# Performance work log

Hardware: AMD Instinct MI355X
Metric: run time of the kernel (lower is better)

## Reference

```python
import jax, jax.numpy as jnp
import numpy as np
from jax.ops import segment_sum

N_NODES = 100000
IN_C, HID_C, OUT_C = 128, 128, 64
N_EDGES = 1600000


def gcn_conv(x, row, col, dinv, W, b):
    # PyG GCNConv: symmetric normalization with self-loops.
    # h = X W; out[c] = sum_{(r,c) in E} dinv[r]*dinv[c]*h[r] + dinv[v]^2*h[v] + b
    h = x @ W  # [N, F_out]
    norm = dinv[row] * dinv[col]  # [E]
    agg = segment_sum(h[row] * norm[:, None], col, num_segments=x.shape[0])
    agg = agg + h * (dinv * dinv)[:, None]  # self-loop contribution
    return agg + b


def setup_inputs() -> dict:
    key = jax.random.key(0)
    k1, k2, k3, k4, k5, k6 = jax.random.split(key, 6)
    x = jax.random.normal(k1, (N_NODES, IN_C), dtype=jnp.float32)
    edge_index = jax.random.randint(k2, (2, N_EDGES), 0, N_NODES, dtype=jnp.int64)
    # Glorot-style init for GCN weights, zero bias (as in PyG GCNConv)
    W1 = jax.random.normal(k3, (IN_C, HID_C), dtype=jnp.float32) / np.sqrt(IN_C)
    b1 = jnp.zeros((HID_C,), dtype=jnp.float32)
    W2 = jax.random.normal(k4, (HID_C, OUT_C), dtype=jnp.float32) / np.sqrt(HID_C)
    b2 = jnp.zeros((OUT_C,), dtype=jnp.float32)
    return {"x": x, "edge_index": edge_index, "W1": W1, "b1": b1, "W2": W2, "b2": b2}


def reference(x, edge_index, W1, b1, W2, b2):
    row, col = edge_index[0], edge_index[1]
    n = x.shape[0]
    # degree counts include self-loop (+1)
    deg = segment_sum(jnp.ones_like(col, dtype=x.dtype), col, num_segments=n) + 1.0
    dinv = jax.lax.rsqrt(deg)
    h = gcn_conv(x, row, col, dinv, W1, b1)
    h = jax.nn.relu(h)
    # dropout is identity in eval mode (get_embedding runs model.eval())
    out = gcn_conv(h, row, col, dinv, W2, b2)
    return out
```

## Files before the change

### kernel.cpp

```cpp
#include <hip/hip_runtime.h>
#include <math.h>


#define BS 256
#define EPB 4096
#define BK_SHIFT 9

typedef __attribute__((ext_vector_type(8))) short bf16x8;
typedef __attribute__((ext_vector_type(4))) float f32x4;

union FragU {
    bf16x8 v;
    unsigned u[4];
};

__device__ __forceinline__ unsigned pack_bf16x2(float a, float b) {
    unsigned ua = __float_as_uint(a);
    unsigned ub = __float_as_uint(b);
    ua = (ua + 0x7fffu + ((ua >> 16) & 1u)) >> 16;
    ub = (ub + 0x7fffu + ((ub >> 16) & 1u)) >> 16;
    return ua | (ub << 16);
}

__device__ __forceinline__ ushort bf16_rte(float a) {
    unsigned ua = __float_as_uint(a);
    return (ushort)((ua + 0x7fffu + ((ua >> 16) & 1u)) >> 16);
}

__device__ __forceinline__ float bf_lo(unsigned u) { return __uint_as_float(u << 16); }
__device__ __forceinline__ float bf_hi(unsigned u) { return __uint_as_float(u & 0xffff0000u); }

__global__ __launch_bounds__(BS) void p1_hist_kernel(const int* __restrict__ col,
                                                     int* __restrict__ countsT,
                                                     int E, int NBUCK, int NBLK) {
    __shared__ int h[256];
    int tid = threadIdx.x;
    h[tid] = 0;
    __syncthreads();
    int e0 = blockIdx.x * EPB;
    int e1 = min(e0 + EPB, E);
    for (int i = e0 + tid; i < e1; i += BS) atomicAdd(&h[col[i] >> BK_SHIFT], 1);
    __syncthreads();
    for (int b = tid; b < NBUCK; b += BS) countsT[b * NBLK + blockIdx.x] = h[b];
}

__global__ __launch_bounds__(BS) void scan_block_kernel(const int* __restrict__ in,
                                                        int* __restrict__ exc,
                                                        int* __restrict__ bsum, int N) {
    __shared__ int s[BS];
    int tid = threadIdx.x;
    int i = blockIdx.x * BS + tid;
    int v = (i < N) ? in[i] : 0;
    s[tid] = v;
    __syncthreads();
    for (int off = 1; off < BS; off <<= 1) {
        int t = (tid >= off) ? s[tid - off] : 0;
        __syncthreads();
        s[tid] += t;
        __syncthreads();
    }
    if (i < N) exc[i] = s[tid] - v;
    if (tid == BS - 1) bsum[blockIdx.x] = s[BS - 1];
}

__global__ __launch_bounds__(512) void scan_bsum_kernel(const int* __restrict__ bsum,
                                                        int* __restrict__ boff, int NB) {
    __shared__ int s[512];
    int tid = threadIdx.x;
    int v = (tid < NB) ? bsum[tid] : 0;
    s[tid] = v;
    __syncthreads();
    for (int off = 1; off < 512; off <<= 1) {
        int t = (tid >= off) ? s[tid - off] : 0;
        __syncthreads();
        s[tid] += t;
        __syncthreads();
    }
    if (tid < NB) boff[tid] = s[tid] - v;
}

__global__ __launch_bounds__(BS) void add_off_kernel(int* __restrict__ exc,
                                                     const int* __restrict__ boff, int N) {
    int i = blockIdx.x * BS + threadIdx.x;
    if (i < N) exc[i] += boff[blockIdx.x];
}

__global__ __launch_bounds__(BS) void p2_scatter_kernel(const int* __restrict__ row,
                                                        const int* __restrict__ col,
                                                        const int* __restrict__ baseT,
                                                        uint2* __restrict__ pairs,
                                                        int E, int NBUCK, int NBLK) {
    __shared__ int cur[256];
    int tid = threadIdx.x;
    for (int b = tid; b < NBUCK; b += BS) cur[b] = baseT[b * NBLK + blockIdx.x];
    __syncthreads();
    int e0 = blockIdx.x * EPB;
    int e1 = min(e0 + EPB, E);
    for (int i = e0 + tid; i < e1; i += BS) {
        int c = col[i];
        int r = row[i];
        int pos = atomicAdd(&cur[c >> BK_SHIFT], 1);
        pairs[pos] = make_uint2((unsigned)r, (unsigned)c);
    }
}

__global__ __launch_bounds__(BS) void p3_build_kernel(const uint2* __restrict__ pairs,
                                                      const int* __restrict__ baseT,
                                                      int* __restrict__ off_g,
                                                      int* __restrict__ deg_g,
                                                      float* __restrict__ dinv,
                                                      int* __restrict__ src,
                                                      int E, int n, int NBUCK, int NBLK) {
    __shared__ int cnt[512];
    __shared__ int scn[512];
    __shared__ int a256[256];
    int tid = threadIdx.x;
    int b = blockIdx.x;
    int s = baseT[b * NBLK];
    int eEnd = (b == NBUCK - 1) ? E : baseT[(b + 1) * NBLK];

    cnt[tid] = 0;
    cnt[tid + 256] = 0;
    __syncthreads();
    for (int i = s + tid; i < eEnd; i += BS) {
        uint2 p = pairs[i];
        atomicAdd(&cnt[p.y & 511], 1);
    }
    __syncthreads();
    int pairsum = cnt[2 * tid] + cnt[2 * tid + 1];
    a256[tid] = pairsum;
    __syncthreads();
    for (int off = 1; off < 256; off <<= 1) {
        int t = (tid >= off) ? a256[tid - off] : 0;
        __syncthreads();
        a256[tid] += t;
        __syncthreads();
    }
    int exc = a256[tid] - pairsum;
    scn[2 * tid] = exc;
    scn[2 * tid + 1] = exc + cnt[2 * tid];
    __syncthreads();
#pragma unroll
    for (int l = tid; l < 512; l += BS) {
        int node = (b << BK_SHIFT) + l;
        if (node < n) {
            off_g[node] = s + scn[l];
            deg_g[node] = cnt[l];
            dinv[node] = rsqrtf((float)(cnt[l] + 1));
        }
    }
    __syncthreads();
#pragma unroll
    for (int l = tid; l < 512; l += BS) scn[l] += s;
    __syncthreads();
    for (int i = s + tid; i < eEnd; i += BS) {
        uint2 p = pairs[i];
        int pos = atomicAdd(&scn[p.y & 511], 1);
        src[pos] = (int)p.x;
    }
}

__global__ __launch_bounds__(BS) void wprep_kernel(const float* __restrict__ W1,
                                                   const float* __restrict__ W2,
                                                   ushort* __restrict__ wt1,
                                                   ushort* __restrict__ wt2) {
    int t = blockIdx.x * BS + threadIdx.x;
    if (t < 128 * 128) {
        int nn = t >> 7, k = t & 127;
        wt1[t] = bf16_rte(W1[k * 128 + nn]);
    }
    if (t < 64 * 128) {
        int nn = t >> 7, k = t & 127;
        wt2[t] = bf16_rte(W2[k * 64 + nn]);
    }
}

template <int NCH, bool IN_BF16>
__global__ __launch_bounds__(BS) void gemm_mfma_kernel(const void* __restrict__ Ain,
                                                       const ushort* __restrict__ WT,
                                                       const float* __restrict__ dinv,
                                                       unsigned* __restrict__ G, int n) {
    constexpr int NT = NCH / 16;
    constexpr int KP = 136;
    __shared__ ushort wlds[NCH * KP];

    int tid = threadIdx.x;
    for (int c = tid; c < NCH * 16; c += BS) {
        int nr = c >> 4, q16 = c & 15;
        *(uint4*)(wlds + nr * KP + q16 * 8) = ((const uint4*)WT)[c];
    }
    __syncthreads();

    int lane = tid & 63, wv = tid >> 6;
    int ml = lane & 15, quad = lane >> 4;
    int m = blockIdx.x * 64 + wv * 16 + ml;

    FragU b[4];
    if (m < n) {
        if (IN_BF16) {
#pragma unroll
            for (int ks = 0; ks < 4; ++ks) {
                uint4 t = ((const uint4*)Ain)[(size_t)m * 16 + ks * 4 + quad];
                b[ks].u[0] = t.x; b[ks].u[1] = t.y; b[ks].u[2] = t.z; b[ks].u[3] = t.w;
            }
        } else {
            const float4* A = (const float4*)Ain + (size_t)m * 32;
#pragma unroll
            for (int ks = 0; ks < 4; ++ks) {
                float4 p0 = A[ks * 8 + quad * 2];
                float4 p1 = A[ks * 8 + quad * 2 + 1];
                b[ks].u[0] = pack_bf16x2(p0.x, p0.y);
                b[ks].u[1] = pack_bf16x2(p0.z, p0.w);
                b[ks].u[2] = pack_bf16x2(p1.x, p1.y);
                b[ks].u[3] = pack_bf16x2(p1.z, p1.w);
            }
        }
    } else {
#pragma unroll
        for (int ks = 0; ks < 4; ++ks) {
            b[ks].u[0] = 0; b[ks].u[1] = 0; b[ks].u[2] = 0; b[ks].u[3] = 0;
        }
    }

    f32x4 acc[NT];
#pragma unroll
    for (int nt = 0; nt < NT; ++nt) {
        acc[nt][0] = 0.f; acc[nt][1] = 0.f; acc[nt][2] = 0.f; acc[nt][3] = 0.f;
    }

#pragma unroll
    for (int nt = 0; nt < NT; ++nt) {
#pragma unroll
        for (int ks = 0; ks < 4; ++ks) {
            bf16x8 a = *(const bf16x8*)(wlds + (nt * 16 + ml) * KP + ks * 32 + quad * 8);
            acc[nt] = __builtin_amdgcn_mfma_f32_16x16x32_bf16(a, b[ks].v, acc[nt], 0, 0, 0);
        }
    }

    if (m < n) {
        float dv = dinv[m];
        unsigned* grow = G + (size_t)m * (NCH / 2);
#pragma unroll
        for (int nt = 0; nt < NT; ++nt) {
            uint2 o;
            o.x = pack_bf16x2(acc[nt][0] * dv, acc[nt][1] * dv);
            o.y = pack_bf16x2(acc[nt][2] * dv, acc[nt][3] * dv);
            *(uint2*)(grow + nt * 8 + quad * 2) = o;
        }
    }
}

template <int C, bool RELU, bool OUT_BF16>
__global__ __launch_bounds__(BS) void agg_kernel(const unsigned* __restrict__ G,
                                                 const int* __restrict__ edge_off,
                                                 const int* __restrict__ cnt,
                                                 const int* __restrict__ src,
                                                 const float* __restrict__ dinv,
                                                 const float* __restrict__ bias,
                                                 void* __restrict__ out, int n) {
    constexpr int Gp = C / 8;
    constexpr int NPB = BS / Gp;
    int lane = threadIdx.x % Gp;
    int li = threadIdx.x / Gp;
    int node = blockIdx.x * NPB + li;
    if (node >= n) return;

    const uint4* G4 = (const uint4*)G;
    float acc[8];
    {
        uint4 sv = G4[(size_t)node * Gp + lane];
        acc[0] = bf_lo(sv.x); acc[1] = bf_hi(sv.x);
        acc[2] = bf_lo(sv.y); acc[3] = bf_hi(sv.y);
        acc[4] = bf_lo(sv.z); acc[5] = bf_hi(sv.z);
        acc[6] = bf_lo(sv.w); acc[7] = bf_hi(sv.w);
    }
    const int* sp = src + edge_off[node];
    int deg = cnt[node];

#define ACCUM(v)                                                               \
    acc[0] += bf_lo(v.x); acc[1] += bf_hi(v.x);                                \
    acc[2] += bf_lo(v.y); acc[3] += bf_hi(v.y);                                \
    acc[4] += bf_lo(v.z); acc[5] += bf_hi(v.z);                                \
    acc[6] += bf_lo(v.w); acc[7] += bf_hi(v.w);

    int i = 0;
    for (; i + 8 <= deg; i += 8) {
        int s0 = sp[i + 0], s1 = sp[i + 1], s2 = sp[i + 2], s3 = sp[i + 3];
        int s4 = sp[i + 4], s5 = sp[i + 5], s6 = sp[i + 6], s7 = sp[i + 7];
        uint4 v0 = G4[(size_t)s0 * Gp + lane];
        uint4 v1 = G4[(size_t)s1 * Gp + lane];
        uint4 v2 = G4[(size_t)s2 * Gp + lane];
        uint4 v3 = G4[(size_t)s3 * Gp + lane];
        uint4 v4 = G4[(size_t)s4 * Gp + lane];
        uint4 v5 = G4[(size_t)s5 * Gp + lane];
        uint4 v6 = G4[(size_t)s6 * Gp + lane];
        uint4 v7 = G4[(size_t)s7 * Gp + lane];
        ACCUM(v0) ACCUM(v1) ACCUM(v2) ACCUM(v3)
        ACCUM(v4) ACCUM(v5) ACCUM(v6) ACCUM(v7)
    }
    for (; i + 2 <= deg; i += 2) {
        int s0 = sp[i + 0], s1 = sp[i + 1];
        uint4 v0 = G4[(size_t)s0 * Gp + lane];
        uint4 v1 = G4[(size_t)s1 * Gp + lane];
        ACCUM(v0) ACCUM(v1)
    }
    if (i < deg) {
        uint4 v0 = G4[(size_t)sp[i] * Gp + lane];
        ACCUM(v0)
    }
#undef ACCUM

    float dv = dinv[node];
    const float4* b4 = (const float4*)bias;
    float4 bl = b4[2 * lane + 0], bh = b4[2 * lane + 1];
    float o0x = acc[0] * dv + bl.x, o0y = acc[1] * dv + bl.y;
    float o0z = acc[2] * dv + bl.z, o0w = acc[3] * dv + bl.w;
    float o1x = acc[4] * dv + bh.x, o1y = acc[5] * dv + bh.y;
    float o1z = acc[6] * dv + bh.z, o1w = acc[7] * dv + bh.w;
    if (RELU) {
        o0x = fmaxf(o0x, 0.f); o0y = fmaxf(o0y, 0.f);
        o0z = fmaxf(o0z, 0.f); o0w = fmaxf(o0w, 0.f);
        o1x = fmaxf(o1x, 0.f); o1y = fmaxf(o1y, 0.f);
        o1z = fmaxf(o1z, 0.f); o1w = fmaxf(o1w, 0.f);
    }
    if (OUT_BF16) {
        uint4 ov;
        ov.x = pack_bf16x2(o0x, o0y);
        ov.y = pack_bf16x2(o0z, o0w);
        ov.z = pack_bf16x2(o1x, o1y);
        ov.w = pack_bf16x2(o1z, o1w);
        ((uint4*)out)[(size_t)node * Gp + lane] = ov;
    } else {
        float4* orow = (float4*)((float*)out + (size_t)node * C);
        orow[2 * lane + 0] = make_float4(o0x, o0y, o0z, o0w);
        orow[2 * lane + 1] = make_float4(o1x, o1y, o1z, o1w);
    }
}

extern "C" void kernel_launch(void* const* d_in, const int* in_sizes, int n_in,
                              void* d_out, int out_size, void* d_ws, size_t ws_size,
                              hipStream_t stream) {
    const float* x  = (const float*)d_in[0];
    const int*   ei = (const int*)d_in[1];
    const float* W1 = (const float*)d_in[2];
    const float* b1 = (const float*)d_in[3];
    const float* W2 = (const float*)d_in[4];
    const float* b2 = (const float*)d_in[5];

    const int IN_C = 128, HID_C = 128;
    int n = in_sizes[0] / IN_C;
    int E = in_sizes[1] / 2;
    const int* row = ei;
    const int* col = ei + E;

    int NBUCK = (n + 511) >> BK_SHIFT;
    int NBLK = (E + EPB - 1) / EPB;
    int M = NBUCK * NBLK;
    int NBS = (M + BS - 1) / BS;

    char* w = (char*)d_ws;
    auto alloc = [&](size_t bytes) {
        void* p = (void*)w;
        w += (bytes + 255) & ~(size_t)255;
        return p;
    };
    int*      countsT = (int*)alloc((size_t)M * 4);
    int*      baseT   = (int*)alloc((size_t)M * 4);
    int*      bsum    = (int*)alloc((size_t)NBS * 4);
    int*      boff    = (int*)alloc((size_t)NBS * 4);
    uint2*    pairs   = (uint2*)alloc((size_t)E * 8);
    int*      src     = (int*)alloc((size_t)E * 4);
    int*      off     = (int*)alloc((size_t)n * 4);
    int*      deg     = (int*)alloc((size_t)n * 4);
    float*    dinv    = (float*)alloc((size_t)n * 4);
    ushort*   wt1     = (ushort*)alloc(128 * 128 * 2);
    ushort*   wt2     = (ushort*)alloc(64 * 128 * 2);
    unsigned* g       = (unsigned*)alloc((size_t)n * HID_C * 2);
    unsigned* h1b     = (unsigned*)alloc((size_t)n * HID_C * 2);

    wprep_kernel<<<64, BS, 0, stream>>>(W1, W2, wt1, wt2);

    p1_hist_kernel<<<NBLK, BS, 0, stream>>>(col, countsT, E, NBUCK, NBLK);
    scan_block_kernel<<<NBS, BS, 0, stream>>>(countsT, baseT, bsum, M);
    scan_bsum_kernel<<<1, 512, 0, stream>>>(bsum, boff, NBS);
    add_off_kernel<<<NBS, BS, 0, stream>>>(baseT, boff, M);
    p2_scatter_kernel<<<NBLK, BS, 0, stream>>>(row, col, baseT, pairs, E, NBUCK, NBLK);
    p3_build_kernel<<<NBUCK, BS, 0, stream>>>(pairs, baseT, off, deg, dinv, src,
                                              E, n, NBUCK, NBLK);

    int gridM = (n + 63) / 64;

    gemm_mfma_kernel<128, false><<<gridM, BS, 0, stream>>>(x, wt1, dinv, g, n);
    agg_kernel<128, true, true><<<(n + 15) / 16, BS, 0, stream>>>(g, off, deg, src,
                                                                  dinv, b1, h1b, n);

    gemm_mfma_kernel<64, true><<<gridM, BS, 0, stream>>>(h1b, wt2, dinv, g, n);
    agg_kernel<64, false, false><<<(n + 31) / 32, BS, 0, stream>>>(g, off, deg, src,
                                                                   dinv, b2, d_out, n);
}
```

Measured before the change: 275.2 us.

## Split each node's edge list across sub-groups in aggregation, reduce with shuffles

The aggregation kernel now gives each destination node 32 threads instead of Gp (16 or 8). Those threads form 2 or 4 sub-groups that walk interleaved slices of the edge list, and the partial sums are combined with cross-lane xor shuffles before one sub-group writes the output. This exposes more independent gathers per node, which shortens the serial per-node loop and balances high- and low-degree nodes better. The cost is more threads per node, extra shuffle reductions, idle lanes for nodes with few edges, and more blocks launched.

```diff
diff --git a/kernel.cpp b/kernel.cpp
--- a/kernel.cpp
+++ b/kernel.cpp
@@ -259,23 +259,32 @@
                                                  const float* __restrict__ bias,
                                                  void* __restrict__ out, int n) {
     constexpr int Gp = C / 8;
-    constexpr int NPB = BS / Gp;
-    int lane = threadIdx.x % Gp;
-    int li = threadIdx.x / Gp;
-    int node = blockIdx.x * NPB + li;
+    constexpr int SUBH = 32 / Gp;
+    constexpr int UN = 16 / SUBH;
+    constexpr int GSH = (Gp == 16) ? 4 : 3;
+
+    int tid = threadIdx.x;
+    int lane = tid & 63;
+    int cl = lane & (Gp - 1);
+    int q = (lane >> GSH) & (SUBH - 1);
+    int node = blockIdx.x * (BS / 32) + (tid >> 5);
     if (node >= n) return;
 
     const uint4* G4 = (const uint4*)G;
+    const int* sp = src + edge_off[node];
+    int deg = cnt[node];
+
     float acc[8];
-    {
-        uint4 sv = G4[(size_t)node * Gp + lane];
+    if (q == 0) {
+        uint4 sv = G4[(size_t)node * Gp + cl];
         acc[0] = bf_lo(sv.x); acc[1] = bf_hi(sv.x);
         acc[2] = bf_lo(sv.y); acc[3] = bf_hi(sv.y);
         acc[4] = bf_lo(sv.z); acc[5] = bf_hi(sv.z);
         acc[6] = bf_lo(sv.w); acc[7] = bf_hi(sv.w);
-    }
-    const int* sp = src + edge_off[node];
-    int deg = cnt[node];
+    } else {
+#pragma unroll
+        for (int k = 0; k < 8; ++k) acc[k] = 0.f;
+    }
 
 #define ACCUM(v)                                                               \
     acc[0] += bf_lo(v.x); acc[1] += bf_hi(v.x);                                \
@@ -284,35 +293,38 @@
     acc[6] += bf_lo(v.w); acc[7] += bf_hi(v.w);
 
     int i = 0;
-    for (; i + 8 <= deg; i += 8) {
-        int s0 = sp[i + 0], s1 = sp[i + 1], s2 = sp[i + 2], s3 = sp[i + 3];
-        int s4 = sp[i + 4], s5 = sp[i + 5], s6 = sp[i + 6], s7 = sp[i + 7];
-        uint4 v0 = G4[(size_t)s0 * Gp + lane];
-        uint4 v1 = G4[(size_t)s1 * Gp + lane];
-        uint4 v2 = G4[(size_t)s2 * Gp + lane];
-        uint4 v3 = G4[(size_t)s3 * Gp + lane];
-        uint4 v4 = G4[(size_t)s4 * Gp + lane];
-        uint4 v5 = G4[(size_t)s5 * Gp + lane];
-        uint4 v6 = G4[(size_t)s6 * Gp + lane];
-        uint4 v7 = G4[(size_t)s7 * Gp + lane];
-        ACCUM(v0) ACCUM(v1) ACCUM(v2) ACCUM(v3)
-        ACCUM(v4) ACCUM(v5) ACCUM(v6) ACCUM(v7)
-    }
-    for (; i + 2 <= deg; i += 2) {
-        int s0 = sp[i + 0], s1 = sp[i + 1];
-        uint4 v0 = G4[(size_t)s0 * Gp + lane];
-        uint4 v1 = G4[(size_t)s1 * Gp + lane];
-        ACCUM(v0) ACCUM(v1)
-    }
-    if (i < deg) {
-        uint4 v0 = G4[(size_t)sp[i] * Gp + lane];
+    for (; i + 16 <= deg; i += 16) {
+        int s[UN];
+#pragma unroll
+        for (int u = 0; u < UN; ++u) s[u] = sp[i + q + SUBH * u];
+        uint4 v[UN];
+#pragma unroll
+        for (int u = 0; u < UN; ++u) v[u] = G4[(size_t)s[u] * Gp + cl];
+#pragma unroll
+        for (int u = 0; u < UN; ++u) { ACCUM(v[u]) }
+    }
+    for (; i + SUBH <= deg; i += SUBH) {
+        int s0 = sp[i + q];
+        uint4 v0 = G4[(size_t)s0 * Gp + cl];
         ACCUM(v0)
     }
+    if (i < deg && q < deg - i) {
+        int s0 = sp[i + q];
+        uint4 v0 = G4[(size_t)s0 * Gp + cl];
+        ACCUM(v0)
+    }
 #undef ACCUM
+
+#pragma unroll
+    for (int k = 0; k < 8; ++k) {
+        if constexpr (SUBH == 4) acc[k] += __shfl_xor(acc[k], 8, 64);
+        acc[k] += __shfl_xor(acc[k], 16, 64);
+    }
+    if (q != 0) return;
 
     float dv = dinv[node];
     const float4* b4 = (const float4*)bias;
-    float4 bl = b4[2 * lane + 0], bh = b4[2 * lane + 1];
+    float4 bl = b4[2 * cl + 0], bh = b4[2 * cl + 1];
     float o0x = acc[0] * dv + bl.x, o0y = acc[1] * dv + bl.y;
     float o0z = acc[2] * dv + bl.z, o0w = acc[3] * dv + bl.w;
     float o1x = acc[4] * dv + bh.x, o1y = acc[5] * dv + bh.y;
@@ -329,11 +341,11 @@
         ov.y = pack_bf16x2(o0z, o0w);
         ov.z = pack_bf16x2(o1x, o1y);
         ov.w = pack_bf16x2(o1z, o1w);
-        ((uint4*)out)[(size_t)node * Gp + lane] = ov;
+        ((uint4*)out)[(size_t)node * Gp + cl] = ov;
     } else {
         float4* orow = (float4*)((float*)out + (size_t)node * C);
-        orow[2 * lane + 0] = make_float4(o0x, o0y, o0z, o0w);
-        orow[2 * lane + 1] = make_float4(o1x, o1y, o1z, o1w);
+        orow[2 * cl + 0] = make_float4(o0x, o0y, o0z, o0w);
+        orow[2 * cl + 1] = make_float4(o1x, o1y, o1z, o1w);
     }
 }
 
@@ -391,10 +403,10 @@
     int gridM = (n + 63) / 64;
 
     gemm_mfma_kernel<128, false><<<gridM, BS, 0, stream>>>(x, wt1, dinv, g, n);
-    agg_kernel<128, true, true><<<(n + 15) / 16, BS, 0, stream>>>(g, off, deg, src,
-                                                                  dinv, b1, h1b, n);
+    agg_kernel<128, true, true><<<(n + 7) / 8, BS, 0, stream>>>(g, off, deg, src,
+                                                                dinv, b1, h1b, n);
 
     gemm_mfma_kernel<64, true><<<gridM, BS, 0, stream>>>(h1b, wt2, dinv, g, n);
-    agg_kernel<64, false, false><<<(n + 31) / 32, BS, 0, stream>>>(g, off, deg, src,
-                                                                   dinv, b2, d_out, n);
-}
+    agg_kernel<64, false, false><<<(n + 7) / 8, BS, 0, stream>>>(g, off, deg, src,
+                                                                 dinv, b2, d_out, n);
+}
```

Result: slower. 291.6 us (+6.0%).
